# Kernel optimization log

Measured on AMD Instinct MI355X. Metric: run time of the kernel, lower is better.

The kernel has to match this reference:

```python
import jax, jax.numpy as jnp
from jax import lax
import numpy as np

B, A, T = 128, 32, 32
HID = 64
DEG = 7
MODES = 25
OUT_FRAMES = 12
NHEAD, DHEAD = 16, 64


def legendre_tmat(out_frames, degree):
    # normalized Legendre basis evaluated at t_n, shape [degree+1, len(t_n)]
    t = np.arange(-6, out_frames + 1, dtype=np.float32)
    t = t / t[-1]
    P = [np.ones_like(t), t]
    for n in range(1, degree):
        P.append(((2 * n + 1) * t * P[n] - n * P[n - 1]) / (n + 1))
    P = np.stack(P[: degree + 1], 0)
    norm = np.sqrt((2 * np.arange(degree + 1) + 1) / 2.0).astype(np.float32)
    return (P * norm[:, None]).astype(np.float32)


def _conv(x, w, stride, pad):
    return lax.conv_general_dilated(x, w, (stride, stride), [(pad, pad), (pad, pad)],
                                    dimension_numbers=("NCHW", "OIHW", "NCHW"))


def _bn(x, g, b, eps=1e-5):
    m = jnp.mean(x, axis=(0, 2, 3), keepdims=True)
    v = jnp.var(x, axis=(0, 2, 3), keepdims=True)
    return (x - m) / jnp.sqrt(v + eps) * g[None, :, None, None] + b[None, :, None, None]


def setup_inputs() -> dict:
    key = jax.random.key(0)
    ks = jax.random.split(key, 32)

    def rn(i, shape, scale=0.05):
        return jax.random.normal(ks[i], shape, dtype=jnp.float32) * scale

    inp = {
        "cnn_feat": rn(0, (B, 1024, 14, 14), 1.0),
        "ego_state": rn(1, (B, T, 5), 1.0),
        "agents_state": rn(2, (B, A, T, 5), 1.0),
        "ego_state_len": jax.random.randint(ks[3], (B,), 0, T),
        "agents_state_len": jax.random.randint(ks[4], (B, A), 0, T),
        "agents_grid_pos": jax.random.randint(ks[5], (B, A, 2), 0, 14),
        "state_fc_W": rn(6, (HID, 5)), "state_fc_b": rn(7, (HID,)),
        "lstm_Wih": rn(8, (4 * HID, HID)), "lstm_Whh": rn(9, (4 * HID, HID)),
        "lstm_bih": rn(10, (4 * HID,)), "lstm_bhh": rn(11, (4 * HID,)),
        "enc_fc_W": rn(12, (HID, HID)), "enc_fc_b": rn(13, (HID,)),
        "conv1_W": rn(14, (512, 1024 + HID, 3, 3)),
        "bn1_g": jnp.ones((512,), jnp.float32), "bn1_b": jnp.zeros((512,), jnp.float32),
        "conv2_W": rn(15, (512, 512, 3, 3)),
        "bn2_g": jnp.ones((512,), jnp.float32), "bn2_b": jnp.zeros((512,), jnp.float32),
        "q_W": rn(16, (NHEAD * DHEAD, 512 + HID)),
        "k_W": rn(17, (NHEAD * DHEAD, 512, 1, 1)),
        "v_W": rn(18, (NHEAD * DHEAD, 512, 1, 1)),
        "attn_out_W": rn(19, (512, NHEAD * DHEAD)), "attn_out_b": rn(20, (512,)),
        "cls_W": rn(21, (MODES, 512 + HID + 512)), "cls_b": rn(22, (MODES,)),
        "dec1_W": rn(23, (256, 512 + HID + 512)), "dec1_b": rn(24, (256,)),
        "dec2_W": rn(25, ((DEG + 1) * 2 * MODES, 256)), "dec2_b": rn(26, ((DEG + 1) * 2 * MODES,)),
    }
    return inp


def reference(cnn_feat, ego_state, agents_state, ego_state_len, agents_state_len,
              agents_grid_pos, state_fc_W, state_fc_b, lstm_Wih, lstm_Whh, lstm_bih,
              lstm_bhh, enc_fc_W, enc_fc_b, conv1_W, bn1_g, bn1_b, conv2_W, bn2_g,
              bn2_b, q_W, k_W, v_W, attn_out_W, attn_out_b, cls_W, cls_b, dec1_W,
              dec1_b, dec2_W, dec2_b):
    Bn, _, Hs, Ws = cnn_feat.shape

    def lstm_encode(seq, lens):
        # seq [N,T,5]; packed-sequence semantics with zero init == take h at step len-1
        N, Tn, _ = seq.shape
        h = seq @ state_fc_W.T + state_fc_b  # [N,T,64]

        def step(carry, xt):
            hh, cc = carry
            g = xt @ lstm_Wih.T + hh @ lstm_Whh.T + lstm_bih + lstm_bhh
            i, f_, gg, o = jnp.split(g, 4, axis=-1)
            cc = jax.nn.sigmoid(f_) * cc + jax.nn.sigmoid(i) * jnp.tanh(gg)
            hh = jax.nn.sigmoid(o) * jnp.tanh(cc)
            return (hh, cc), hh

        z = jnp.zeros((N, HID), h.dtype)
        _, hs = lax.scan(step, (z, z), h.transpose(1, 0, 2))  # hs [T,N,64]
        idx = jnp.clip(lens, 1, Tn).astype(jnp.int32) - 1
        last = hs[idx, jnp.arange(N)]
        return last @ enc_fc_W.T + enc_fc_b

    ego = lstm_encode(ego_state, ego_state_len)  # [B,64]
    ag = lstm_encode(agents_state.reshape(Bn * A, T, 5),
                     agents_state_len.reshape(-1)).reshape(Bn, A, HID)

    # scatter-add agent encodings into the spatial grid (overlapping writes accumulate)
    grid = jnp.zeros((Bn, Hs, Ws, HID), cnn_feat.dtype)
    bidx = jnp.broadcast_to(jnp.arange(Bn)[:, None], (Bn, A))
    grid = grid.at[bidx, agents_grid_pos[..., 0], agents_grid_pos[..., 1]].add(ag)

    x = jnp.concatenate([cnn_feat, grid.transpose(0, 3, 1, 2)], axis=1)
    x = jax.nn.relu(_bn(_conv(x, conv1_W, 1, 1), bn1_g, bn1_b))
    x = jax.nn.relu(_bn(_conv(x, conv2_W, 2, 1), bn2_g, bn2_b))  # [B,512,7,7]

    ego_t = jnp.concatenate([x[:, :, 3, 3], ego], axis=1)  # [B,576]
    q = (ego_t @ q_W.T).reshape(Bn, NHEAD, DHEAD)
    k = _conv(x, k_W, 1, 1).reshape(Bn, NHEAD, DHEAD, -1)  # g = 9*9 = 81
    v = _conv(x, v_W, 1, 1).reshape(Bn, NHEAD, DHEAD, -1)
    energy = jnp.einsum("bhf,bhfg->bhg", q, k)
    attn = jax.nn.softmax(energy / (NHEAD * DHEAD) ** 0.5, axis=2)
    o = jnp.einsum("bhg,bhdg->bhd", attn, v).reshape(Bn, -1)
    o = o @ attn_out_W.T + attn_out_b

    feat = jnp.concatenate([o, ego_t], axis=1)  # [B,1088]
    conf = feat @ cls_W.T + cls_b
    d = jax.nn.relu(feat @ dec1_W.T + dec1_b)
    d = (d @ dec2_W.T + dec2_b).reshape(Bn, MODES, -1)

    tmat = jnp.asarray(legendre_tmat(OUT_FRAMES, DEG))  # [DEG+1, 19]
    out_x = d[:, :, : DEG + 1] @ tmat
    out_y = d[:, :, DEG + 1:] @ tmat
    traj = jnp.stack([out_x, out_y], axis=3)  # [B,MODES,19,2]
    return traj, conf
```

## Files before the change

kernel.cpp:

```cpp
#include <hip/hip_runtime.h>
#include <stdint.h>
#include <stddef.h>

#define DEVINL static __device__ __forceinline__

typedef __attribute__((ext_vector_type(8))) short  bfrag;
typedef __attribute__((ext_vector_type(4))) float  facc;

DEVINL uint16_t f2b(float f){
  uint32_t u = __float_as_uint(f);
  return (uint16_t)((u + 0x7fffu + ((u >> 16) & 1u)) >> 16);
}
DEVINL float b2f(uint16_t b){ return __uint_as_float(((uint32_t)b) << 16); }

DEVINL facc MFMA(bfrag a, bfrag b, facc c){
  return __builtin_amdgcn_mfma_f32_16x16x32_bf16(a, b, c, 0, 0, 0);
}

DEVINL void gload16(const void* g, void* l){
  __builtin_amdgcn_global_load_lds(
      (const __attribute__((address_space(1))) uint32_t*)g,
      (__attribute__((address_space(3))) uint32_t*)l, 16, 0, 0);
}

DEVINL float fast_tanh(float x){
  return 2.f/(1.f+__expf(-2.f*x)) - 1.f;
}

struct F2BJobs {
  const float* s[7];
  uint16_t*    d[7];
  int          n[7];
};
__global__ void k_f2b_multi(F2BJobs jobs){
  int j = blockIdx.y;
  const float* s = jobs.s[j];
  uint16_t* d = jobs.d[j];
  int n = jobs.n[j];
  int i = blockIdx.x*256 + threadIdx.x;
  int st = gridDim.x*256;
  for(; i<n; i+=st) d[i] = f2b(s[i]);
}

__global__ void k_zborder(uint16_t* __restrict__ X, uint16_t* __restrict__ Y){
  int b = blockIdx.x & 127, t = threadIdx.x;
  uint16_t* base = (blockIdx.x < 128) ? X : Y;
  int C = (blockIdx.x < 128) ? 1088 : 512;
  for(int p=0;p<60;p++){
    int y, x;
    if(p<16){ y=0; x=p; }
    else if(p<32){ y=15; x=p-16; }
    else { int q=p-32; y=1+(q>>1); x=(q&1)?15:0; }
    uint32_t* dst = (uint32_t*)(base + ((size_t)(b*16+y)*16 + x)*C);
    for(int i=t;i<C/2;i+=256) dst[i] = 0;
  }
}

__global__ void k_lstm_prep(const float* __restrict__ Wih, const float* __restrict__ Whh,
                            const float* __restrict__ bih, const float* __restrict__ bhh,
                            const float* __restrict__ sW, const float* __restrict__ sb,
                            const float* __restrict__ encW,
                            uint16_t* __restrict__ Wc, float* __restrict__ be,
                            uint16_t* __restrict__ encWb, float* __restrict__ tm){
  int n = threadIdx.x;
  if(n < 19){
    float tv = (float)(n - 6) / 12.0f;
    float Pm = 1.0f, Pc = tv;
    tm[0*19+n] = Pm * sqrtf(0.5f);
    tm[1*19+n] = Pc * sqrtf(1.5f);
    for(int q=1; q<7; q++){
      float Pn = ((float)(2*q+1)*tv*Pc - (float)q*Pm) / (float)(q+1);
      Pm = Pc; Pc = Pn;
      tm[(q+1)*19+n] = Pc * sqrtf((float)(2*(q+1)+1) * 0.5f);
    }
  }
  for(int k=0;k<64;k++) Wc[n*96+k] = f2b(Whh[n*64+k]);
  for(int k5=0;k5<5;k5++){
    float s = 0.f;
    for(int j=0;j<64;j++) s += Wih[n*64+j]*sW[j*5+k5];
    Wc[n*96+64+k5] = f2b(s);
  }
  for(int k=69;k<96;k++) Wc[n*96+k] = 0;
  float s = 0.f;
  for(int j=0;j<64;j++) s += Wih[n*64+j]*sb[j];
  be[n] = s + bih[n] + bhh[n];
  if(n < 64){
    for(int k=0;k<64;k++) encWb[n*64+k] = f2b(encW[n*64+k]);
  }
}

__global__ __launch_bounds__(256) void k_lstm(
    const float* __restrict__ ego_seq, const float* __restrict__ ag_seq,
    const int* __restrict__ ego_len, const int* __restrict__ ag_len,
    const int* __restrict__ grid_pos,
    const uint16_t* __restrict__ Wc, const float* __restrict__ be,
    const uint16_t* __restrict__ encWb, const float* __restrict__ encB,
    float* __restrict__ agrid, uint16_t* __restrict__ egoT, uint16_t* __restrict__ feat)
{
  __shared__ __align__(16) uint16_t A[32*96];
  __shared__ float Xf[32*160];
  __shared__ int   idxs[32];

  int t = threadIdx.x, w = t>>6, l = t&63;
  int blk = blockIdx.x;
  bool isEgo = blk < 4;
  int seq0 = isEgo ? blk*32 : (blk-4)*32;
  const float* seqp = (isEgo ? ego_seq : ag_seq) + (size_t)seq0*160;

  for(int i=t;i<32*160;i+=256) Xf[i] = seqp[i];
  if(t < 32){
    int L = isEgo ? ego_len[seq0+t] : ag_len[seq0+t];
    if(L < 1) L = 1;
    idxs[t] = L-1;
  }
  for(int i=t;i<32*96;i+=256) A[i] = 0;

  bfrag bf[4][3];
  float be4[4];
  for(int ct=0;ct<4;ct++){
    int n = (ct*4+w)*16 + (l&15);
    for(int ks=0;ks<3;ks++)
      bf[ct][ks] = *(const bfrag*)(Wc + n*96 + ks*32 + (l>>4)*8);
    be4[ct] = be[n];
  }
  float cst[8], hl[8];
  for(int i=0;i<8;i++){ cst[i]=0.f; hl[i]=0.f; }
  __syncthreads();
  int myidx[8];
  for(int rt=0;rt<2;rt++) for(int r=0;r<4;r++){
    int s = rt*16 + (l>>4)*4 + r;
    myidx[rt*4+r] = idxs[s];
  }

  for(int st=0; st<32; st++){
    if(t < 160){ int s=t/5, kk=t%5; A[s*96+64+kk] = f2b(Xf[s*160 + st*5 + kk]); }
    __syncthreads();
    facc acc[2][4];
    for(int rt=0;rt<2;rt++) for(int ct=0;ct<4;ct++) acc[rt][ct] = facc{0.f,0.f,0.f,0.f};
    #pragma unroll
    for(int ks=0;ks<3;ks++){
      bfrag aA[2];
      #pragma unroll
      for(int rt=0;rt<2;rt++)
        aA[rt] = *(const bfrag*)(A + (rt*16+(l&15))*96 + ks*32 + (l>>4)*8);
      #pragma unroll
      for(int rt=0;rt<2;rt++)
        #pragma unroll
        for(int ct=0;ct<4;ct++)
          acc[rt][ct] = MFMA(aA[rt], bf[ct][ks], acc[rt][ct]);
    }
    __syncthreads();
    #pragma unroll
    for(int rt=0;rt<2;rt++) for(int r=0;r<4;r++){
      int cell = rt*4+r;
      int s = rt*16 + (l>>4)*4 + r;
      float gi = acc[rt][0][r] + be4[0];
      float gf = acc[rt][1][r] + be4[1];
      float gg = acc[rt][2][r] + be4[2];
      float go = acc[rt][3][r] + be4[3];
      float si = 1.f/(1.f+__expf(-gi));
      float sf = 1.f/(1.f+__expf(-gf));
      float so = 1.f/(1.f+__expf(-go));
      float tg = fast_tanh(gg);
      float c2 = sf*cst[cell] + si*tg;
      cst[cell] = c2;
      float hn = so*fast_tanh(c2);
      A[s*96 + w*16 + (l&15)] = f2b(hn);
      if(st == myidx[cell]) hl[cell] = hn;
    }
  }
  __syncthreads();
  for(int rt=0;rt<2;rt++) for(int r=0;r<4;r++){
    int s = rt*16 + (l>>4)*4 + r;
    A[s*96 + w*16 + (l&15)] = f2b(hl[rt*4+r]);
  }
  __syncthreads();
  bfrag eb[2];
  for(int ks=0;ks<2;ks++)
    eb[ks] = *(const bfrag*)(encWb + (w*16+(l&15))*64 + ks*32 + (l>>4)*8);
  facc ea[2]; ea[0] = facc{0.f,0.f,0.f,0.f}; ea[1] = facc{0.f,0.f,0.f,0.f};
  for(int ks=0;ks<2;ks++){
    for(int rt=0;rt<2;rt++){
      bfrag aA = *(const bfrag*)(A + (rt*16+(l&15))*96 + ks*32 + (l>>4)*8);
      ea[rt] = MFMA(aA, eb[ks], ea[rt]);
    }
  }
  int n = w*16 + (l&15);
  float bn_ = encB[n];
  for(int rt=0;rt<2;rt++) for(int r=0;r<4;r++){
    int s = rt*16 + (l>>4)*4 + r;
    float v = ea[rt][r] + bn_;
    int gs = seq0 + s;
    if(isEgo){
      egoT[(size_t)gs*576 + 512 + n] = f2b(v);
      feat[(size_t)gs*1088 + 1024 + n] = f2b(v);
    } else {
      int py = grid_pos[gs*2+0], px = grid_pos[gs*2+1];
      atomicAdd(&agrid[((size_t)(gs>>5)*196 + py*14 + px)*64 + n], v);
    }
  }
}

__global__ void k_packx(const float* __restrict__ cnn, const float* __restrict__ agrid,
                        uint16_t* __restrict__ Xp)
{
  __shared__ float tile[32*200];
  int b = blockIdx.x, ch = blockIdx.y, t = threadIdx.x;
  if(ch < 32){
    int c0 = ch*32;
    for(int i=t;i<32*196;i+=256){
      int ci = i/196, s = i%196;
      tile[ci*200+s] = cnn[((size_t)b*1024 + c0+ci)*196 + s];
    }
    __syncthreads();
    for(int i=t;i<32*196;i+=256){
      int s = i>>5, ci = i&31;
      int y = s/14, x = s%14;
      Xp[(((size_t)b*16 + y+1)*16 + x+1)*1088 + c0 + ci] = f2b(tile[ci*200+s]);
    }
  } else {
    int j0 = (ch-32)*32;
    for(int i=t;i<32*196;i+=256){
      int s = i>>5, ji = i&31;
      int y = s/14, x = s%14;
      Xp[(((size_t)b*16 + y+1)*16 + x+1)*1088 + 1024 + j0 + ji] =
          f2b(agrid[((size_t)b*196 + s)*64 + j0 + ji]);
    }
  }
}

__global__ void k_packw(const float* __restrict__ W, uint16_t* __restrict__ Wp, int O, int C)
{
  int o = blockIdx.x;
  int c = blockIdx.y*64 + threadIdx.x;
  const float* src = W + ((size_t)o*C + c)*9;
  float v[9];
  #pragma unroll
  for(int d=0;d<9;d++) v[d] = src[d];
  #pragma unroll
  for(int d=0;d<9;d++)
    Wp[((size_t)d*O + o)*C + c] = f2b(v[d]);
}

__global__ void k_packw2(const float* __restrict__ W, uint16_t* __restrict__ Wp)
{
  int o = blockIdx.x;
  int c = blockIdx.y*64 + threadIdx.x;
  const float* src = W + ((size_t)o*512 + c)*9;
  float v[9];
  #pragma unroll
  for(int d=0;d<9;d++) v[d] = src[d];
  #pragma unroll
  for(int dy=0;dy<3;dy++)
    #pragma unroll
    for(int dx=0;dx<3;dx++)
      Wp[((size_t)(dy*512 + o))*1536 + dx*512 + c] = f2b(v[dy*3+dx]);
}

__global__ __launch_bounds__(512) void k_conv1_8p(
    const uint16_t* __restrict__ Ain, const uint16_t* __restrict__ Wb,
    uint16_t* __restrict__ Out, float* __restrict__ stats)
{
  constexpr int CB = 1088;
  constexpr int NSTEP = 153;
  __shared__ __align__(16) char LDSb[131072];

  int t = threadIdx.x, w = t>>6, l = t&63;
  int wm = w>>2, wn = w&3;

  int xcd = blockIdx.x & 7, pos = blockIdx.x >> 3;
  int wgid = (xcd < 4 ? xcd*25 : 100 + (xcd-4)*24) + pos;
  int m0 = (wgid % 98) * 256;
  int n0 = (wgid / 98) * 256;

  const uint16_t* aP[2][2];
  const uint16_t* bP[2][2];
  #pragma unroll
  for(int P=0;P<2;P++)
    #pragma unroll
    for(int j=0;j<2;j++){
      int partrow = j*64 + (t>>3);
      int swz = ((t&7) ^ (partrow&7))*8;
      int gr = P*64 + partrow + ((partrow>=64)?64:0);
      int m = m0 + gr; int b = m/196, s = m%196, y = s/14, x = s%14;
      aP[P][j] = Ain + ((b*16+y)*16+x)*CB + swz;
      int nb = n0 + (partrow>>5)*64 + P*32 + (partrow&31);
      bP[P][j] = Wb + (size_t)nb*CB + swz;
    }

  facc acc[8][4];
  #pragma unroll
  for(int i=0;i<8;i++)
    #pragma unroll
    for(int j=0;j<4;j++) acc[i][j] = facc{0.f,0.f,0.f,0.f};

  bfrag aF[4][2], bF[2][2];
  int dd = 0;

  #define STG(buf, PART) do{                                                   \
    if((PART)==0 || (PART)==3){ const int P_ = ((PART)==3);                    \
      _Pragma("unroll")                                                        \
      for(int j_=0;j_<2;j_++)                                                  \
        gload16(aP[P_][j_], LDSb + (buf)*65536 + P_*16384 + j_*8192 + w*1024); \
    } else { const int P_ = ((PART)==2);                                       \
      _Pragma("unroll")                                                        \
      for(int j_=0;j_<2;j_++)                                                  \
        gload16(bP[P_][j_], LDSb + (buf)*65536 + 32768 + P_*16384 + j_*8192 + w*1024); \
    }                                                                          \
  }while(0)

  #define ADVK() do{                                                          \
    if(dd==8){                                                                \
      _Pragma("unroll")                                                       \
      for(int P_=0;P_<2;P_++) for(int j_=0;j_<2;j_++){                        \
        aP[P_][j_] += 64 - 34*CB; bP[P_][j_] += 64 - 8*512*CB; }              \
      dd = 0;                                                                 \
    } else {                                                                  \
      int sA_ = (dd==2||dd==5) ? 14*CB : CB;                                  \
      _Pragma("unroll")                                                       \
      for(int P_=0;P_<2;P_++) for(int j_=0;j_<2;j_++){                        \
        aP[P_][j_] += sA_; bP[P_][j_] += 512*CB; }                            \
      dd++;                                                                   \
    }                                                                         \
  }while(0)

  #define VM4 asm volatile("s_waitcnt vmcnt(4)" ::: "memory")
  #define VM2 asm volatile("s_waitcnt vmcnt(2)" ::: "memory")
  #define VM0 asm volatile("s_waitcnt vmcnt(0)" ::: "memory")

  #define LDA(mh) do{                                                         \
    const uint16_t* Ab_ = (const uint16_t*)(LDSb + p*65536 + (mh)*16384);     \
    _Pragma("unroll")                                                         \
    for(int i_=0;i_<4;i_++)                                                   \
      _Pragma("unroll")                                                       \
      for(int ks_=0;ks_<2;ks_++)                                              \
        aF[i_][ks_] = *(const bfrag*)(Ab_ + (wm*64 + i_*16 + (l&15))*64       \
                        + ((ks_*32 + (l>>4)*8) ^ ((l&7)<<3)));                \
  }while(0)

  #define LDB(nh) do{                                                         \
    const uint16_t* Bb_ = (const uint16_t*)(LDSb + p*65536 + 32768 + (nh)*16384); \
    _Pragma("unroll")                                                         \
    for(int j_=0;j_<2;j_++)                                                   \
      _Pragma("unroll")                                                       \
      for(int ks_=0;ks_<2;ks_++)                                              \
        bF[j_][ks_] = *(const bfrag*)(Bb_ + (wn*32 + j_*16 + (l&15))*64       \
                        + ((ks_*32 + (l>>4)*8) ^ ((l&7)<<3)));                \
  }while(0)

  #define MM(mh, nh) do{                                                      \
    __builtin_amdgcn_s_setprio(1);                                            \
    _Pragma("unroll")                                                         \
    for(int ks_=0;ks_<2;ks_++)                                                \
      _Pragma("unroll")                                                       \
      for(int i_=0;i_<4;i_++)                                                 \
        _Pragma("unroll")                                                     \
        for(int j_=0;j_<2;j_++)                                               \
          acc[(mh)*4+i_][(nh)*2+j_] =                                         \
            MFMA(aF[i_][ks_], bF[j_][ks_], acc[(mh)*4+i_][(nh)*2+j_]);        \
    __builtin_amdgcn_s_setprio(0);                                            \
  }while(0)

  #define BARS do{ __builtin_amdgcn_sched_barrier(0); __builtin_amdgcn_s_barrier(); }while(0)
  #define EBAR __builtin_amdgcn_s_barrier()

  STG(0,0); STG(0,1); STG(0,2); STG(0,3);
  ADVK();
  VM4;
  EBAR;

  for(int kt=0; kt<NSTEP-1; kt++){
    int p = kt&1;
    LDA(0); LDB(0); STG(p^1,0); BARS; MM(0,0); VM4; EBAR;
    LDB(1);         STG(p^1,1); BARS; MM(0,1); VM4; EBAR;
    LDA(1);         STG(p^1,2); BARS; MM(1,1);      EBAR;
    LDB(0);         STG(p^1,3); BARS; MM(1,0); VM4; EBAR;
    if(kt < NSTEP-2) ADVK();
  }
  {
    int p = 0;
    LDA(0); LDB(0); BARS; MM(0,0); VM2; EBAR;
    LDB(1);         BARS; MM(0,1); VM0; EBAR;
    LDA(1);         BARS; MM(1,1);      EBAR;
    LDB(0);         BARS; MM(1,0);      EBAR;
  }

  #undef LDA
  #undef LDB
  #undef MM
  #undef BARS
  #undef EBAR
  #undef STG
  #undef ADVK

  __syncthreads();
  int* oo = (int*)LDSb;
  if(t < 256){
    int m = m0 + t; int b = m/196, s = m%196, y = s/14, x = s%14;
    oo[t] = ((b*16 + y+1)*16 + (x+1))*512;
  }
  __syncthreads();
  #pragma unroll
  for(int i=0;i<8;i++)
    #pragma unroll
    for(int j=0;j<4;j++){
      int n = n0 + wn*64 + j*16 + (l&15);
      #pragma unroll
      for(int r=0;r<4;r++){
        int mr = wm*128 + i*16 + (l>>4)*4 + r;
        Out[(size_t)oo[mr] + n] = f2b(acc[i][j][r]);
      }
    }
  __syncthreads();
  float* sred = (float*)LDSb;
  int rg = wm*4 + (l>>4);
  #pragma unroll
  for(int j=0;j<4;j++){
    float s=0.f, q=0.f;
    #pragma unroll
    for(int i=0;i<8;i++)
      #pragma unroll
      for(int r=0;r<4;r++){ float v = acc[i][j][r]; s += v; q += v*v; }
    int nl = wn*64 + j*16 + (l&15);
    sred[(nl*8 + rg)*2+0] = s;
    sred[(nl*8 + rg)*2+1] = q;
  }
  __syncthreads();
  if(t < 256){
    float s=0.f, q=0.f;
    #pragma unroll
    for(int rgi=0;rgi<8;rgi++){ s += sred[(t*8+rgi)*2]; q += sred[(t*8+rgi)*2+1]; }
    atomicAdd(&stats[n0+t], s);
    atomicAdd(&stats[512+n0+t], q);
  }
}

__global__ __launch_bounds__(256) void k_conv2dy(
    const uint16_t* __restrict__ Ain, const uint16_t* __restrict__ Wb,
    float* __restrict__ PS)
{
  __shared__ __align__(16) uint16_t As[128*64];
  __shared__ __align__(16) uint16_t Bs[128*64];

  int t = threadIdx.x, w = t>>6, l = t&63;
  int dy = blockIdx.y;

  int xcd = blockIdx.x & 7, pos = blockIdx.x >> 3;
  int wgid = (xcd < 4 ? xcd*25 : 100 + (xcd-4)*24) + pos;
  int n0 = (wgid / 49) * 128;
  int m0 = (wgid % 49) * 128;

  const uint16_t* aP[4];
  const uint16_t* bP[4];
  #pragma unroll
  for(int p=0;p<4;p++){
    int r = w*32 + p*8 + (l>>3);
    int m = m0 + r;
    int b = m/49, s = m%49, y = s/7, x = s%7;
    aP[p] = Ain + ((b*16 + 2*y + dy)*16 + 2*x)*512 + (l&7)*8;
    bP[p] = Wb + ((size_t)(dy*512 + n0 + r))*1536 + (l&7)*8;
  }

  facc acc[4][4];
  #pragma unroll
  for(int i=0;i<4;i++)
    #pragma unroll
    for(int j=0;j<4;j++) acc[i][j] = facc{0.f,0.f,0.f,0.f};
  int wm = w>>1, wn = w&1;
  char* asDst = (char*)As + w*4096;
  char* bsDst = (char*)Bs + w*4096;

  for(int stp=0; stp<24; stp++){
    #pragma unroll
    for(int p=0;p<4;p++){ gload16(aP[p], asDst + p*1024); aP[p] += 64; }
    #pragma unroll
    for(int p=0;p<4;p++){ gload16(bP[p], bsDst + p*1024); bP[p] += 64; }
    __syncthreads();
    #pragma unroll
    for(int ks=0;ks<2;ks++){
      bfrag a[4], b[4];
      #pragma unroll
      for(int i=0;i<4;i++)
        a[i] = *(const bfrag*)(As + (wm*64 + i*16 + (l&15))*64 + ks*32 + (l>>4)*8);
      #pragma unroll
      for(int j=0;j<4;j++)
        b[j] = *(const bfrag*)(Bs + (wn*64 + j*16 + (l&15))*64 + ks*32 + (l>>4)*8);
      #pragma unroll
      for(int i=0;i<4;i++)
        #pragma unroll
        for(int j=0;j<4;j++)
          acc[i][j] = MFMA(a[i], b[j], acc[i][j]);
    }
    __syncthreads();
  }

  float* out = PS + (size_t)dy*3211264;
  #pragma unroll
  for(int i=0;i<4;i++)
    #pragma unroll
    for(int j=0;j<4;j++){
      int n = n0 + wn*64 + j*16 + (l&15);
      #pragma unroll
      for(int r=0;r<4;r++){
        int mr = m0 + wm*64 + i*16 + (l>>4)*4 + r;
        out[(size_t)mr*512 + n] = acc[i][j][r];
      }
    }
}

__global__ void k_bn2sum(const float* __restrict__ PS, uint16_t* __restrict__ Y2,
                         float* __restrict__ stats)
{
  int t = threadIdx.x;
  int m0 = blockIdx.x*16;
  float s0=0,s1=0,q0=0,q1=0;
  for(int i=0;i<16;i++){
    size_t off = (size_t)(m0+i)*512 + 2*t;
    float2 p0 = *(const float2*)(PS + off);
    float2 p1 = *(const float2*)(PS + 3211264 + off);
    float2 p2 = *(const float2*)(PS + 6422528 + off);
    float a = p0.x+p1.x+p2.x, c = p0.y+p1.y+p2.y;
    s0+=a; q0+=a*a; s1+=c; q1+=c*c;
    *(uint32_t*)(Y2 + off) = (uint32_t)f2b(a) | ((uint32_t)f2b(c)<<16);
  }
  atomicAdd(&stats[2*t],   s0);
  atomicAdd(&stats[2*t+1], s1);
  atomicAdd(&stats[512+2*t],   q0);
  atomicAdd(&stats[512+2*t+1], q1);
}

__global__ __launch_bounds__(256) void k_convkv(
    const uint16_t* __restrict__ Ain, const uint16_t* __restrict__ Wb,
    uint16_t* __restrict__ Out)
{
  constexpr int CB = 512;
  constexpr int NWG = 49*16;
  constexpr int Q8 = NWG/8;

  __shared__ __align__(16) uint16_t As[128*64];
  __shared__ __align__(16) uint16_t Bs[128*64];

  int t = threadIdx.x, w = t>>6, l = t&63;

  int xcd = blockIdx.x & 7, pos = blockIdx.x >> 3;
  int wgid = xcd*Q8 + pos;
  int n0 = (wgid / 49) * 128;
  int m0 = (wgid % 49) * 128;

  const uint16_t* aP[4];
  const uint16_t* bP[4];
  #pragma unroll
  for(int p=0;p<4;p++){
    int r = w*32 + p*8 + (l>>3);
    aP[p] = Ain + (size_t)(m0 + r)*512 + (l&7)*8;
    bP[p] = Wb + (size_t)(n0 + r)*CB + (l&7)*8;
  }

  facc acc[4][4];
  #pragma unroll
  for(int i=0;i<4;i++)
    #pragma unroll
    for(int j=0;j<4;j++) acc[i][j] = facc{0.f,0.f,0.f,0.f};
  int wm = w>>1, wn = w&1;
  char* asDst = (char*)As + w*4096;
  char* bsDst = (char*)Bs + w*4096;

  for(int cc=0; cc<8; cc++){
    #pragma unroll
    for(int p=0;p<4;p++){ gload16(aP[p], asDst + p*1024); aP[p] += 64; }
    #pragma unroll
    for(int p=0;p<4;p++){ gload16(bP[p], bsDst + p*1024); bP[p] += 64; }
    __syncthreads();
    #pragma unroll
    for(int ks=0;ks<2;ks++){
      bfrag a[4], b[4];
      #pragma unroll
      for(int i=0;i<4;i++)
        a[i] = *(const bfrag*)(As + (wm*64 + i*16 + (l&15))*64 + ks*32 + (l>>4)*8);
      #pragma unroll
      for(int j=0;j<4;j++)
        b[j] = *(const bfrag*)(Bs + (wn*64 + j*16 + (l&15))*64 + ks*32 + (l>>4)*8);
      #pragma unroll
      for(int i=0;i<4;i++)
        #pragma unroll
        for(int j=0;j<4;j++)
          acc[i][j] = MFMA(a[i], b[j], acc[i][j]);
    }
    __syncthreads();
  }

  #pragma unroll
  for(int i=0;i<4;i++)
    #pragma unroll
    for(int j=0;j<4;j++){
      int n = n0 + wn*64 + j*16 + (l&15);
      #pragma unroll
      for(int r=0;r<4;r++){
        int mr = m0 + wm*64 + i*16 + (l>>4)*4 + r;
        Out[(size_t)mr*2048 + n] = f2b(acc[i][j][r]);
      }
    }
}

template<int PAD>
__global__ void k_bnapply(uint16_t* __restrict__ Y, const float* __restrict__ stats,
                          const float* __restrict__ gg, const float* __restrict__ bb,
                          int M, float invM,
                          uint16_t* __restrict__ egoT, uint16_t* __restrict__ feat)
{
  int t = threadIdx.x;
  int m0 = blockIdx.x*8;
  float mu0 = stats[2*t]*invM,       mu1 = stats[2*t+1]*invM;
  float v0 = stats[512+2*t]*invM - mu0*mu0, v1 = stats[512+2*t+1]*invM - mu1*mu1;
  float sc0 = gg[2*t]  *rsqrtf(v0+1e-5f), sc1 = gg[2*t+1]*rsqrtf(v1+1e-5f);
  float sh0 = bb[2*t]   - mu0*sc0,        sh1 = bb[2*t+1] - mu1*sc1;
  for(int i=0;i<8;i++){
    int m = m0+i; if(m>=M) break;
    size_t off;
    if(PAD){ int b=m/196, s=m%196, y=s/14, x=s%14; off = (((size_t)b*16+y+1)*16 + x+1)*512; }
    else off = (size_t)m*512;
    uint32_t u = *(const uint32_t*)(Y + off + 2*t);
    float a = fmaxf(b2f((uint16_t)u)*sc0 + sh0, 0.f);
    float c = fmaxf(b2f((uint16_t)(u>>16))*sc1 + sh1, 0.f);
    uint32_t pu = (uint32_t)f2b(a) | ((uint32_t)f2b(c)<<16);
    *(uint32_t*)(Y + off + 2*t) = pu;
    if(!PAD && (m%49)==24){
      int b = m/49;
      *(uint32_t*)(egoT + (size_t)b*576 + 2*t) = pu;
      *(uint32_t*)(feat + (size_t)b*1088 + 512 + 2*t) = pu;
    }
  }
}

__global__ __launch_bounds__(256) void k_sgemm(
    const uint16_t* __restrict__ A, int lda,
    const uint16_t* __restrict__ B, int ldb,
    const float* __restrict__ bias,
    void* __restrict__ C, int ldc,
    int N, int K, int flags)
{
  int t = threadIdx.x, w = t>>6, l = t&63;
  int nt = blockIdx.x*4 + w;
  int n  = nt*16 + (l&15);
  int m0 = blockIdx.y*16;
  bool nv = n < N;
  facc acc = facc{0.f,0.f,0.f,0.f};
  for(int k=0;k<K;k+=32){
    bfrag af = *(const bfrag*)(A + (size_t)(m0+(l&15))*lda + k + (l>>4)*8);
    bfrag bf_ = {0,0,0,0,0,0,0,0};
    if(nv) bf_ = *(const bfrag*)(B + (size_t)n*ldb + k + (l>>4)*8);
    acc = MFMA(af, bf_, acc);
  }
  if(nv){
    float bv = bias ? bias[n] : 0.f;
    #pragma unroll
    for(int r=0;r<4;r++){
      int m = m0 + (l>>4)*4 + r;
      float v = acc[r] + bv;
      if(flags & 1) v = fmaxf(v, 0.f);
      if(flags & 2) ((float*)C)[(size_t)m*ldc + n] = v;
      else ((uint16_t*)C)[(size_t)m*ldc + n] = f2b(v);
    }
  }
}

__global__ __launch_bounds__(256) void k_attn(
    const float* __restrict__ q, const uint16_t* __restrict__ kv,
    uint16_t* __restrict__ o)
{
  int t = threadIdx.x, w = t>>6, l = t&63;
  int idx = blockIdx.x*4 + w;
  int b = idx>>4, h = idx&15;
  float qf = q[(size_t)b*1024 + h*64 + l];
  const uint16_t* kp = kv + (size_t)b*49*2048 + h*64 + l;
  float eo = 0.f;
  for(int g=0; g<49; g++){
    float p = qf * b2f(kp[(size_t)g*2048]);
    for(int s=32;s>0;s>>=1) p += __shfl_xor(p, s);
    if(l == g) eo = p;
  }
  float e = (l<49) ? eo*(1.f/32.f) : -1e30f;
  float mx = e;
  for(int s=32;s>0;s>>=1) mx = fmaxf(mx, __shfl_xor(mx, s));
  mx = fmaxf(mx, 0.f);
  float p = (l<49) ? __expf(e-mx) : 0.f;
  float den = p;
  for(int s=32;s>0;s>>=1) den += __shfl_xor(den, s);
  den += 32.f*__expf(-mx);
  const uint16_t* vp = kv + (size_t)b*49*2048 + 1024 + h*64 + l;
  float accv = 0.f;
  for(int g=0; g<49; g++){
    float pg = __shfl(p, g);
    accv += pg * b2f(vp[(size_t)g*2048]);
  }
  o[(size_t)b*1024 + h*64 + l] = f2b(accv/den);
}

__global__ void k_traj(const float* __restrict__ d2, const float* __restrict__ tm,
                       float* __restrict__ out)
{
  int i = blockIdx.x*256 + threadIdx.x;
  if(i >= 3200) return;
  const float* dp = d2 + (size_t)i*16;
  float cx[8], cy[8];
  #pragma unroll
  for(int j=0;j<8;j++){ cx[j]=dp[j]; cy[j]=dp[8+j]; }
  float* op = out + (size_t)i*38;
  for(int tt=0;tt<19;tt++){
    float x=0.f, y=0.f;
    #pragma unroll
    for(int j=0;j<8;j++){ float tv = tm[j*19+tt]; x += cx[j]*tv; y += cy[j]*tv; }
    op[tt*2+0]=x; op[tt*2+1]=y;
  }
}

extern "C" void kernel_launch(void* const* d_in, const int* in_sizes, int n_in,
                              void* d_out, int out_size, void* d_ws, size_t ws_size,
                              hipStream_t stream)
{
  const float* cnn      = (const float*)d_in[0];
  const float* ego_seq  = (const float*)d_in[1];
  const float* ag_seq   = (const float*)d_in[2];
  const int*   ego_len  = (const int*)d_in[3];
  const int*   ag_len   = (const int*)d_in[4];
  const int*   grid_pos = (const int*)d_in[5];
  const float* sW  = (const float*)d_in[6];
  const float* sb  = (const float*)d_in[7];
  const float* Wih = (const float*)d_in[8];
  const float* Whh = (const float*)d_in[9];
  const float* bih = (const float*)d_in[10];
  const float* bhh = (const float*)d_in[11];
  const float* encW = (const float*)d_in[12];
  const float* encB = (const float*)d_in[13];
  const float* conv1W = (const float*)d_in[14];
  const float* bn1g = (const float*)d_in[15];
  const float* bn1b = (const float*)d_in[16];
  const float* conv2W = (const float*)d_in[17];
  const float* bn2g = (const float*)d_in[18];
  const float* bn2b = (const float*)d_in[19];
  const float* qWf  = (const float*)d_in[20];
  const float* kWf  = (const float*)d_in[21];
  const float* vWf  = (const float*)d_in[22];
  const float* aoW  = (const float*)d_in[23];
  const float* aoB  = (const float*)d_in[24];
  const float* clsWf = (const float*)d_in[25];
  const float* clsB  = (const float*)d_in[26];
  const float* d1Wf  = (const float*)d_in[27];
  const float* d1B   = (const float*)d_in[28];
  const float* d2Wf  = (const float*)d_in[29];
  const float* d2B   = (const float*)d_in[30];

  char* ws = (char*)d_ws;
  const size_t XP_OFF   = 0;
  const size_t PS_OFF   = 0;
  const size_t KV_OFF   = 0;
  const size_t Y2_OFF   = 41943040;
  const size_t Y1P_OFF  = 71303168;
  const size_t WP1_OFF  = 104857600;
  const size_t WP2_OFF  = 114884608;
  const size_t WKV_OFF  = 119603200;
  const size_t QW_OFF   = 121700352;
  const size_t AOW_OFF  = 122880000;
  const size_t CLSW_OFF = 123928576;
  const size_t D1W_OFF  = 123982976;
  const size_t D2W_OFF  = 124540032;
  const size_t GRID_OFF = 124744832;
  const size_t EGOT_OFF = 131167360;
  const size_t FEAT_OFF = 131314816;
  const size_t QBUF_OFF = 131593344;
  const size_t OBUF_OFF = 132117632;
  const size_t D1_OFF   = 132379776;
  const size_t D2_OFF   = 132445312;
  const size_t WC_OFF   = 132650112;
  const size_t BE_OFF   = 132699264;
  const size_t ENCW_OFF = 132700288;
  const size_t TMAT_OFF = 132708480;
  const size_t ST1_OFF  = 132709120;
  const size_t ST2_OFF  = 132713216;

  uint16_t* XP   = (uint16_t*)(ws + XP_OFF);
  float*    PS   = (float*)(ws + PS_OFF);
  uint16_t* KV   = (uint16_t*)(ws + KV_OFF);
  uint16_t* Y2   = (uint16_t*)(ws + Y2_OFF);
  uint16_t* Y1P  = (uint16_t*)(ws + Y1P_OFF);
  uint16_t* WP1  = (uint16_t*)(ws + WP1_OFF);
  uint16_t* WP2  = (uint16_t*)(ws + WP2_OFF);
  uint16_t* WKV  = (uint16_t*)(ws + WKV_OFF);
  uint16_t* QW   = (uint16_t*)(ws + QW_OFF);
  uint16_t* AOW  = (uint16_t*)(ws + AOW_OFF);
  uint16_t* CLSW = (uint16_t*)(ws + CLSW_OFF);
  uint16_t* D1W  = (uint16_t*)(ws + D1W_OFF);
  uint16_t* D2W  = (uint16_t*)(ws + D2W_OFF);
  float*    GRIDB= (float*)(ws + GRID_OFF);
  uint16_t* EGOT = (uint16_t*)(ws + EGOT_OFF);
  uint16_t* FEAT = (uint16_t*)(ws + FEAT_OFF);
  float*    QBUF = (float*)(ws + QBUF_OFF);
  uint16_t* OBUF = (uint16_t*)(ws + OBUF_OFF);
  uint16_t* D1B  = (uint16_t*)(ws + D1_OFF);
  float*    D2B  = (float*)(ws + D2_OFF);
  uint16_t* WC   = (uint16_t*)(ws + WC_OFF);
  float*    BE   = (float*)(ws + BE_OFF);
  uint16_t* ENCWB= (uint16_t*)(ws + ENCW_OFF);
  float*    TMAT = (float*)(ws + TMAT_OFF);
  float*    ST1  = (float*)(ws + ST1_OFF);
  float*    ST2  = (float*)(ws + ST2_OFF);
  float*    outF = (float*)d_out;

  (void)hipMemsetAsync(ws + GRID_OFF, 0, 6422528, stream);
  (void)hipMemsetAsync(ws + ST1_OFF,  0, 8192, stream);

  k_zborder<<<256,256,0,stream>>>(XP, Y1P);

  k_lstm_prep<<<1,256,0,stream>>>(Wih,Whh,bih,bhh,sW,sb,encW, WC,BE,ENCWB, TMAT);
  k_packw<<<dim3(512,17),64,0,stream>>>(conv1W, WP1, 512, 1088);
  k_packw2<<<dim3(512,8),64,0,stream>>>(conv2W, WP2);
  {
    F2BJobs jb;
    jb.s[0]=kWf;  jb.d[0]=WKV;              jb.n[0]=1024*512;
    jb.s[1]=vWf;  jb.d[1]=WKV + 1024*512;   jb.n[1]=1024*512;
    jb.s[2]=qWf;  jb.d[2]=QW;               jb.n[2]=1024*576;
    jb.s[3]=aoW;  jb.d[3]=AOW;              jb.n[3]=512*1024;
    jb.s[4]=clsWf;jb.d[4]=CLSW;             jb.n[4]=25*1088;
    jb.s[5]=d1Wf; jb.d[5]=D1W;              jb.n[5]=256*1088;
    jb.s[6]=d2Wf; jb.d[6]=D2W;              jb.n[6]=400*256;
    k_f2b_multi<<<dim3(48,7),256,0,stream>>>(jb);
  }

  k_lstm<<<132,256,0,stream>>>(ego_seq, ag_seq, ego_len, ag_len, grid_pos,
                               WC, BE, ENCWB, encB, GRIDB, EGOT, FEAT);
  k_packx<<<dim3(128,34),256,0,stream>>>(cnn, GRIDB, XP);
  k_conv1_8p<<<196,512,0,stream>>>(XP, WP1, Y1P, ST1);
  k_bnapply<1><<<3136,256,0,stream>>>(Y1P, ST1, bn1g, bn1b, 25088, 1.f/25088.f, nullptr, nullptr);
  k_conv2dy<<<dim3(196,3),256,0,stream>>>(Y1P, WP2, PS);
  k_bn2sum<<<392,256,0,stream>>>(PS, Y2, ST2);
  k_bnapply<0><<<784,256,0,stream>>>(Y2, ST2, bn2g, bn2b, 6272, 1.f/6272.f, EGOT, FEAT);
  k_convkv<<<784,256,0,stream>>>(Y2, WKV, KV);
  k_sgemm<<<dim3(16,8),256,0,stream>>>(EGOT, 576, QW, 576, nullptr, QBUF, 1024, 1024, 576, 2);
  k_attn<<<512,256,0,stream>>>(QBUF, KV, OBUF);
  k_sgemm<<<dim3(8,8),256,0,stream>>>(OBUF, 1024, AOW, 1024, aoB, FEAT, 1088, 512, 1024, 0);
  k_sgemm<<<dim3(1,8),256,0,stream>>>(FEAT, 1088, CLSW, 1088, clsB, outF + 121600, 25, 25, 1088, 2);
  k_sgemm<<<dim3(4,8),256,0,stream>>>(FEAT, 1088, D1W, 1088, d1B, D1B, 256, 256, 1088, 1);
  k_sgemm<<<dim3(7,8),256,0,stream>>>(D1B, 256, D2W, 256, d2B, D2B, 400, 400, 256, 2);
  k_traj<<<13,256,0,stream>>>(D2B, TMAT, outF);

  (void)in_sizes; (void)n_in; (void)out_size; (void)ws_size;
}
```

Before: 629.6 us.

## Fold K/V projections into query and output via associativity, drop KV conv

Instead of computing full K and V 1x1 convolutions over all 49 positions (a 6272x2048x512 GEMM), the query is first projected through the per-head K weights to get a 512-dim vector per head. Energies are then dot products with the raw conv2 features. The attention-weighted sum of raw features is then projected through the V weights per head. This removes the large KV GEMM and its intermediate buffer, at the cost of two small batched GEMMs and a new attention kernel that stages each batch's features in LDS. Separately, conv1 keeps both B fragment halves in registers so the fourth sub-step no longer reloads B from LDS.

```diff
diff --git a/kernel.cpp b/kernel.cpp
--- a/kernel.cpp
+++ b/kernel.cpp
@@ -28,9 +28,9 @@
 }
 
 struct F2BJobs {
-  const float* s[7];
-  uint16_t*    d[7];
-  int          n[7];
+  const float* s[6];
+  uint16_t*    d[6];
+  int          n[6];
 };
 __global__ void k_f2b_multi(F2BJobs jobs){
   int j = blockIdx.y;
@@ -257,6 +257,18 @@
       Wp[((size_t)(dy*512 + o))*1536 + dx*512 + c] = f2b(v[dy*3+dx]);
 }
 
+__global__ void k_packwk(const float* __restrict__ kW, uint16_t* __restrict__ WKT)
+{
+  int h = blockIdx.x;
+  int c0 = blockIdx.y*32;
+  int t = threadIdx.x;
+  int d = t & 63;
+  for(int ci = t>>6; ci<32; ci+=4){
+    int c = c0 + ci;
+    WKT[((size_t)h*512 + c)*64 + d] = f2b(kW[((size_t)(h*64+d))*512 + c]);
+  }
+}
+
 __global__ __launch_bounds__(512) void k_conv1_8p(
     const uint16_t* __restrict__ Ain, const uint16_t* __restrict__ Wb,
     uint16_t* __restrict__ Out, float* __restrict__ stats)
@@ -294,7 +306,7 @@
     #pragma unroll
     for(int j=0;j<4;j++) acc[i][j] = facc{0.f,0.f,0.f,0.f};
 
-  bfrag aF[4][2], bF[2][2];
+  bfrag aF[4][2], bF0[2][2], bF1[2][2];
   int dd = 0;
 
   #define STG(buf, PART) do{                                                   \
@@ -338,27 +350,27 @@
                         + ((ks_*32 + (l>>4)*8) ^ ((l&7)<<3)));                \
   }while(0)
 
-  #define LDB(nh) do{                                                         \
+  #define LDB(dst, nh) do{                                                   \
     const uint16_t* Bb_ = (const uint16_t*)(LDSb + p*65536 + 32768 + (nh)*16384); \
     _Pragma("unroll")                                                         \
     for(int j_=0;j_<2;j_++)                                                   \
       _Pragma("unroll")                                                       \
       for(int ks_=0;ks_<2;ks_++)                                              \
-        bF[j_][ks_] = *(const bfrag*)(Bb_ + (wn*32 + j_*16 + (l&15))*64       \
+        dst[j_][ks_] = *(const bfrag*)(Bb_ + (wn*32 + j_*16 + (l&15))*64      \
                         + ((ks_*32 + (l>>4)*8) ^ ((l&7)<<3)));                \
   }while(0)
 
-  #define MM(mh, nh) do{                                                      \
-    __builtin_amdgcn_s_setprio(1);                                            \
-    _Pragma("unroll")                                                         \
-    for(int ks_=0;ks_<2;ks_++)                                                \
-      _Pragma("unroll")                                                       \
-      for(int i_=0;i_<4;i_++)                                                 \
-        _Pragma("unroll")                                                     \
-        for(int j_=0;j_<2;j_++)                                               \
-          acc[(mh)*4+i_][(nh)*2+j_] =                                         \
-            MFMA(aF[i_][ks_], bF[j_][ks_], acc[(mh)*4+i_][(nh)*2+j_]);        \
-    __builtin_amdgcn_s_setprio(0);                                            \
+  #define MM(mh, nh, bsrc) do{                                               \
+    __builtin_amdgcn_s_setprio(1);                                           \
+    _Pragma("unroll")                                                        \
+    for(int ks_=0;ks_<2;ks_++)                                               \
+      _Pragma("unroll")                                                      \
+      for(int i_=0;i_<4;i_++)                                                \
+        _Pragma("unroll")                                                    \
+        for(int j_=0;j_<2;j_++)                                              \
+          acc[(mh)*4+i_][(nh)*2+j_] =                                        \
+            MFMA(aF[i_][ks_], bsrc[j_][ks_], acc[(mh)*4+i_][(nh)*2+j_]);     \
+    __builtin_amdgcn_s_setprio(0);                                           \
   }while(0)
 
   #define BARS do{ __builtin_amdgcn_sched_barrier(0); __builtin_amdgcn_s_barrier(); }while(0)
@@ -371,18 +383,18 @@
 
   for(int kt=0; kt<NSTEP-1; kt++){
     int p = kt&1;
-    LDA(0); LDB(0); STG(p^1,0); BARS; MM(0,0); VM4; EBAR;
-    LDB(1);         STG(p^1,1); BARS; MM(0,1); VM4; EBAR;
-    LDA(1);         STG(p^1,2); BARS; MM(1,1);      EBAR;
-    LDB(0);         STG(p^1,3); BARS; MM(1,0); VM4; EBAR;
+    LDA(0); LDB(bF0,0); STG(p^1,0); BARS; MM(0,0,bF0); VM4; EBAR;
+    LDB(bF1,1);         STG(p^1,1); BARS; MM(0,1,bF1); VM4; EBAR;
+    LDA(1);             STG(p^1,2); BARS; MM(1,1,bF1);      EBAR;
+                        STG(p^1,3); BARS; MM(1,0,bF0); VM4; EBAR;
     if(kt < NSTEP-2) ADVK();
   }
   {
     int p = 0;
-    LDA(0); LDB(0); BARS; MM(0,0); VM2; EBAR;
-    LDB(1);         BARS; MM(0,1); VM0; EBAR;
-    LDA(1);         BARS; MM(1,1);      EBAR;
-    LDB(0);         BARS; MM(1,0);      EBAR;
+    LDA(0); LDB(bF0,0); BARS; MM(0,0,bF0); VM2; EBAR;
+    LDB(bF1,1);         BARS; MM(0,1,bF1); VM0; EBAR;
+    LDA(1);             BARS; MM(1,1,bF1);      EBAR;
+                        BARS; MM(1,0,bF0);      EBAR;
   }
 
   #undef LDA
@@ -527,79 +539,6 @@
   atomicAdd(&stats[2*t+1], s1);
   atomicAdd(&stats[512+2*t],   q0);
   atomicAdd(&stats[512+2*t+1], q1);
-}
-
-__global__ __launch_bounds__(256) void k_convkv(
-    const uint16_t* __restrict__ Ain, const uint16_t* __restrict__ Wb,
-    uint16_t* __restrict__ Out)
-{
-  constexpr int CB = 512;
-  constexpr int NWG = 49*16;
-  constexpr int Q8 = NWG/8;
-
-  __shared__ __align__(16) uint16_t As[128*64];
-  __shared__ __align__(16) uint16_t Bs[128*64];
-
-  int t = threadIdx.x, w = t>>6, l = t&63;
-
-  int xcd = blockIdx.x & 7, pos = blockIdx.x >> 3;
-  int wgid = xcd*Q8 + pos;
-  int n0 = (wgid / 49) * 128;
-  int m0 = (wgid % 49) * 128;
-
-  const uint16_t* aP[4];
-  const uint16_t* bP[4];
-  #pragma unroll
-  for(int p=0;p<4;p++){
-    int r = w*32 + p*8 + (l>>3);
-    aP[p] = Ain + (size_t)(m0 + r)*512 + (l&7)*8;
-    bP[p] = Wb + (size_t)(n0 + r)*CB + (l&7)*8;
-  }
-
-  facc acc[4][4];
-  #pragma unroll
-  for(int i=0;i<4;i++)
-    #pragma unroll
-    for(int j=0;j<4;j++) acc[i][j] = facc{0.f,0.f,0.f,0.f};
-  int wm = w>>1, wn = w&1;
-  char* asDst = (char*)As + w*4096;
-  char* bsDst = (char*)Bs + w*4096;
-
-  for(int cc=0; cc<8; cc++){
-    #pragma unroll
-    for(int p=0;p<4;p++){ gload16(aP[p], asDst + p*1024); aP[p] += 64; }
-    #pragma unroll
-    for(int p=0;p<4;p++){ gload16(bP[p], bsDst + p*1024); bP[p] += 64; }
-    __syncthreads();
-    #pragma unroll
-    for(int ks=0;ks<2;ks++){
-      bfrag a[4], b[4];
-      #pragma unroll
-      for(int i=0;i<4;i++)
-        a[i] = *(const bfrag*)(As + (wm*64 + i*16 + (l&15))*64 + ks*32 + (l>>4)*8);
-      #pragma unroll
-      for(int j=0;j<4;j++)
-        b[j] = *(const bfrag*)(Bs + (wn*64 + j*16 + (l&15))*64 + ks*32 + (l>>4)*8);
-      #pragma unroll
-      for(int i=0;i<4;i++)
-        #pragma unroll
-        for(int j=0;j<4;j++)
-          acc[i][j] = MFMA(a[i], b[j], acc[i][j]);
-    }
-    __syncthreads();
-  }
-
-  #pragma unroll
-  for(int i=0;i<4;i++)
-    #pragma unroll
-    for(int j=0;j<4;j++){
-      int n = n0 + wn*64 + j*16 + (l&15);
-      #pragma unroll
-      for(int r=0;r<4;r++){
-        int mr = m0 + wm*64 + i*16 + (l>>4)*4 + r;
-        Out[(size_t)mr*2048 + n] = f2b(acc[i][j][r]);
-      }
-    }
 }
 
 template<int PAD>
@@ -664,22 +603,64 @@
   }
 }
 
-__global__ __launch_bounds__(256) void k_attn(
-    const float* __restrict__ q, const uint16_t* __restrict__ kv,
-    uint16_t* __restrict__ o)
+__global__ __launch_bounds__(256) void k_bgemm(
+    const uint16_t* __restrict__ A, int lda, int aoffs,
+    const uint16_t* __restrict__ B, int ldb, int brows,
+    uint16_t* __restrict__ C, int ldc, int coffs,
+    int K)
 {
   int t = threadIdx.x, w = t>>6, l = t&63;
-  int idx = blockIdx.x*4 + w;
-  int b = idx>>4, h = idx&15;
-  float qf = q[(size_t)b*1024 + h*64 + l];
-  const uint16_t* kp = kv + (size_t)b*49*2048 + h*64 + l;
-  float eo = 0.f;
-  for(int g=0; g<49; g++){
-    float p = qf * b2f(kp[(size_t)g*2048]);
-    for(int s=32;s>0;s>>=1) p += __shfl_xor(p, s);
-    if(l == g) eo = p;
-  }
-  float e = (l<49) ? eo*(1.f/32.f) : -1e30f;
+  int z = blockIdx.z;
+  int n = (blockIdx.x*4 + w)*16 + (l&15);
+  int m0 = blockIdx.y*16;
+  const uint16_t* Ab = A + (size_t)z*aoffs;
+  const uint16_t* Bb = B + (size_t)z*brows*ldb;
+  facc acc = facc{0.f,0.f,0.f,0.f};
+  for(int k=0;k<K;k+=32){
+    bfrag af = *(const bfrag*)(Ab + (size_t)(m0+(l&15))*lda + k + (l>>4)*8);
+    bfrag bf_ = *(const bfrag*)(Bb + (size_t)n*ldb + k + (l>>4)*8);
+    acc = MFMA(af, bf_, acc);
+  }
+  #pragma unroll
+  for(int r=0;r<4;r++){
+    int m = m0 + (l>>4)*4 + r;
+    C[(size_t)m*ldc + z*coffs + n] = f2b(acc[r]);
+  }
+}
+
+__global__ __launch_bounds__(512) void k_attn2(
+    const uint16_t* __restrict__ U16, const uint16_t* __restrict__ y2,
+    uint16_t* __restrict__ zout)
+{
+  __shared__ __align__(16) char LA[49*1024 + 8*1024];
+  uint16_t* uls = (uint16_t*)(LA + 49*1024);
+  int t = threadIdx.x, w = t>>6, l = t&63;
+  int b = blockIdx.x >> 1, half = blockIdx.x & 1;
+  int h = half*8 + w;
+
+  for(int i=t; i<3136; i+=512){
+    int g = i>>6, c16 = i&63;
+    *(uint4*)(LA + g*1024 + ((c16*16) ^ ((g&31)<<4))) =
+        *(const uint4*)(y2 + ((size_t)(b*49+g)*512 + c16*8));
+  }
+  *(uint4*)((char*)uls + w*1024 + l*16) =
+      *(const uint4*)(U16 + (size_t)b*8192 + h*512 + l*8);
+  __syncthreads();
+
+  float dot = 0.f;
+  if(l < 49){
+    const char* yrow = LA + l*1024;
+    const char* ur = (const char*)uls + w*1024;
+    for(int c16=0;c16<64;c16++){
+      uint4 uv = *(const uint4*)(ur + c16*16);
+      uint4 yv = *(const uint4*)(yrow + ((c16*16) ^ ((l&31)<<4)));
+      const uint16_t* up = (const uint16_t*)&uv;
+      const uint16_t* yp = (const uint16_t*)&yv;
+      #pragma unroll
+      for(int j=0;j<8;j++) dot += b2f(up[j])*b2f(yp[j]);
+    }
+  }
+  float e = (l<49) ? dot*(1.f/32.f) : -1e30f;
   float mx = e;
   for(int s=32;s>0;s>>=1) mx = fmaxf(mx, __shfl_xor(mx, s));
   mx = fmaxf(mx, 0.f);
@@ -687,13 +668,22 @@
   float den = p;
   for(int s=32;s>0;s>>=1) den += __shfl_xor(den, s);
   den += 32.f*__expf(-mx);
-  const uint16_t* vp = kv + (size_t)b*49*2048 + 1024 + h*64 + l;
-  float accv = 0.f;
+
+  float z[8];
+  #pragma unroll
+  for(int j=0;j<8;j++) z[j]=0.f;
   for(int g=0; g<49; g++){
     float pg = __shfl(p, g);
-    accv += pg * b2f(vp[(size_t)g*2048]);
-  }
-  o[(size_t)b*1024 + h*64 + l] = f2b(accv/den);
+    uint4 yv = *(const uint4*)(LA + g*1024 + ((l*16) ^ ((g&31)<<4)));
+    const uint16_t* yp = (const uint16_t*)&yv;
+    #pragma unroll
+    for(int j=0;j<8;j++) z[j] += pg*b2f(yp[j]);
+  }
+  float inv = 1.f/den;
+  uint16_t zr[8];
+  #pragma unroll
+  for(int j=0;j<8;j++) zr[j] = f2b(z[j]*inv);
+  *(uint4*)(zout + ((size_t)(b*16+h)*512) + l*8) = *(uint4*)zr;
 }
 
 __global__ void k_traj(const float* __restrict__ d2, const float* __restrict__ tm,
@@ -753,12 +743,14 @@
   char* ws = (char*)d_ws;
   const size_t XP_OFF   = 0;
   const size_t PS_OFF   = 0;
-  const size_t KV_OFF   = 0;
+  const size_t U_OFF    = 0;
+  const size_t ZB_OFF   = 2097152;
   const size_t Y2_OFF   = 41943040;
   const size_t Y1P_OFF  = 71303168;
   const size_t WP1_OFF  = 104857600;
   const size_t WP2_OFF  = 114884608;
-  const size_t WKV_OFF  = 119603200;
+  const size_t WKT_OFF  = 119603200;
+  const size_t WVB_OFF  = 120651776;
   const size_t QW_OFF   = 121700352;
   const size_t AOW_OFF  = 122880000;
   const size_t CLSW_OFF = 123928576;
@@ -767,7 +759,7 @@
   const size_t GRID_OFF = 124744832;
   const size_t EGOT_OFF = 131167360;
   const size_t FEAT_OFF = 131314816;
-  const size_t QBUF_OFF = 131593344;
+  const size_t QB_OFF   = 131593344;
   const size_t OBUF_OFF = 132117632;
   const size_t D1_OFF   = 132379776;
   const size_t D2_OFF   = 132445312;
@@ -780,12 +772,14 @@
 
   uint16_t* XP   = (uint16_t*)(ws + XP_OFF);
   float*    PS   = (float*)(ws + PS_OFF);
-  uint16_t* KV   = (uint16_t*)(ws + KV_OFF);
+  uint16_t* U16  = (uint16_t*)(ws + U_OFF);
+  uint16_t* ZB16 = (uint16_t*)(ws + ZB_OFF);
   uint16_t* Y2   = (uint16_t*)(ws + Y2_OFF);
   uint16_t* Y1P  = (uint16_t*)(ws + Y1P_OFF);
   uint16_t* WP1  = (uint16_t*)(ws + WP1_OFF);
   uint16_t* WP2  = (uint16_t*)(ws + WP2_OFF);
-  uint16_t* WKV  = (uint16_t*)(ws + WKV_OFF);
+  uint16_t* WKT  = (uint16_t*)(ws + WKT_OFF);
+  uint16_t* WVB  = (uint16_t*)(ws + WVB_OFF);
   uint16_t* QW   = (uint16_t*)(ws + QW_OFF);
   uint16_t* AOW  = (uint16_t*)(ws + AOW_OFF);
   uint16_t* CLSW = (uint16_t*)(ws + CLSW_OFF);
@@ -794,7 +788,7 @@
   float*    GRIDB= (float*)(ws + GRID_OFF);
   uint16_t* EGOT = (uint16_t*)(ws + EGOT_OFF);
   uint16_t* FEAT = (uint16_t*)(ws + FEAT_OFF);
-  float*    QBUF = (float*)(ws + QBUF_OFF);
+  uint16_t* QB16 = (uint16_t*)(ws + QB_OFF);
   uint16_t* OBUF = (uint16_t*)(ws + OBUF_OFF);
   uint16_t* D1B  = (uint16_t*)(ws + D1_OFF);
   float*    D2B  = (float*)(ws + D2_OFF);
@@ -814,16 +808,16 @@
   k_lstm_prep<<<1,256,0,stream>>>(Wih,Whh,bih,bhh,sW,sb,encW, WC,BE,ENCWB, TMAT);
   k_packw<<<dim3(512,17),64,0,stream>>>(conv1W, WP1, 512, 1088);
   k_packw2<<<dim3(512,8),64,0,stream>>>(conv2W, WP2);
+  k_packwk<<<dim3(16,16),256,0,stream>>>(kWf, WKT);
   {
     F2BJobs jb;
-    jb.s[0]=kWf;  jb.d[0]=WKV;              jb.n[0]=1024*512;
-    jb.s[1]=vWf;  jb.d[1]=WKV + 1024*512;   jb.n[1]=1024*512;
-    jb.s[2]=qWf;  jb.d[2]=QW;               jb.n[2]=1024*576;
-    jb.s[3]=aoW;  jb.d[3]=AOW;              jb.n[3]=512*1024;
-    jb.s[4]=clsWf;jb.d[4]=CLSW;             jb.n[4]=25*1088;
-    jb.s[5]=d1Wf; jb.d[5]=D1W;              jb.n[5]=256*1088;
-    jb.s[6]=d2Wf; jb.d[6]=D2W;              jb.n[6]=400*256;
-    k_f2b_multi<<<dim3(48,7),256,0,stream>>>(jb);
+    jb.s[0]=vWf;  jb.d[0]=WVB;   jb.n[0]=1024*512;
+    jb.s[1]=qWf;  jb.d[1]=QW;    jb.n[1]=1024*576;
+    jb.s[2]=aoW;  jb.d[2]=AOW;   jb.n[2]=512*1024;
+    jb.s[3]=clsWf;jb.d[3]=CLSW;  jb.n[3]=25*1088;
+    jb.s[4]=d1Wf; jb.d[4]=D1W;   jb.n[4]=256*1088;
+    jb.s[5]=d2Wf; jb.d[5]=D2W;   jb.n[5]=400*256;
+    k_f2b_multi<<<dim3(48,6),256,0,stream>>>(jb);
   }
 
   k_lstm<<<132,256,0,stream>>>(ego_seq, ag_seq, ego_len, ag_len, grid_pos,
@@ -834,9 +828,10 @@
   k_conv2dy<<<dim3(196,3),256,0,stream>>>(Y1P, WP2, PS);
   k_bn2sum<<<392,256,0,stream>>>(PS, Y2, ST2);
   k_bnapply<0><<<784,256,0,stream>>>(Y2, ST2, bn2g, bn2b, 6272, 1.f/6272.f, EGOT, FEAT);
-  k_convkv<<<784,256,0,stream>>>(Y2, WKV, KV);
-  k_sgemm<<<dim3(16,8),256,0,stream>>>(EGOT, 576, QW, 576, nullptr, QBUF, 1024, 1024, 576, 2);
-  k_attn<<<512,256,0,stream>>>(QBUF, KV, OBUF);
+  k_sgemm<<<dim3(16,8),256,0,stream>>>(EGOT, 576, QW, 576, nullptr, QB16, 1024, 1024, 576, 0);
+  k_bgemm<<<dim3(8,8,16),256,0,stream>>>(QB16, 1024, 64, WKT, 64, 512, U16, 8192, 512, 64);
+  k_attn2<<<256,512,0,stream>>>(U16, Y2, ZB16);
+  k_bgemm<<<dim3(1,8,16),256,0,stream>>>(ZB16, 8192, 512, WVB, 512, 64, OBUF, 1024, 64, 512);
   k_sgemm<<<dim3(8,8),256,0,stream>>>(OBUF, 1024, AOW, 1024, aoB, FEAT, 1088, 512, 1024, 0);
   k_sgemm<<<dim3(1,8),256,0,stream>>>(FEAT, 1088, CLSW, 1088, clsB, outF + 121600, 25, 25, 1088, 2);
   k_sgemm<<<dim3(4,8),256,0,stream>>>(FEAT, 1088, D1W, 1088, d1B, D1B, 256, 256, 1088, 1);
```

Measured after the change: 599.0 us. 1.05x faster.
